# Performance work log

Hardware: AMD Instinct MI355X
Metric: run time of the kernel (lower is better)

Reference implementation:

```python
import jax, jax.numpy as jnp
import numpy as np

B, S, H, NH = 2, 2048, 1024, 16
HD = H // NH  # 64


def setup_inputs() -> dict:
    key = jax.random.key(0)
    ks = jax.random.split(key, 11)
    sc = 1.0 / np.sqrt(H)
    inp = {
        "q": jax.random.normal(ks[0], (B, S, H), dtype=jnp.float32),
        "k": jax.random.normal(ks[1], (B, S, H), dtype=jnp.float32),
        "v": jax.random.normal(ks[2], (B, S, H), dtype=jnp.float32),
        # nn.Linear params: weight [out,in], bias [out]
        "wq_w": jax.random.normal(ks[3], (H, H), dtype=jnp.float32) * sc,
        "wq_b": jnp.zeros((H,), dtype=jnp.float32),
        "wk_w": jax.random.normal(ks[4], (H, H), dtype=jnp.float32) * sc,
        "wk_b": jnp.zeros((H,), dtype=jnp.float32),
        "wv_w": jax.random.normal(ks[5], (H, H), dtype=jnp.float32) * sc,
        "wv_b": jnp.zeros((H,), dtype=jnp.float32),
        "wo_w": jax.random.normal(ks[6], (H, H), dtype=jnp.float32) * sc,
        "wo_b": jnp.zeros((H,), dtype=jnp.float32),
    }
    return inp


def _split_heads(x):
    # [B,S,H] -> [B,NH,S,HD]
    b, s, _ = x.shape
    return x.reshape(b, s, NH, HD).transpose(0, 2, 1, 3)


def reference(q, k, v, wq_w, wq_b, wk_w, wk_b, wv_w, wv_b, wo_w, wo_b):
    qw = q @ wq_w.T + wq_b
    kw = k @ wk_w.T + wk_b
    vw = v @ wv_w.T + wv_b
    hq = _split_heads(qw)  # [B,NH,S,HD]
    hk = _split_heads(kw)
    hv = _split_heads(vw)
    scale = 1.0 / jnp.sqrt(jnp.float32(HD))
    scores = jnp.einsum("bhqd,bhkd->bhqk", hq, hk) * scale  # [B,NH,S,S]
    attn = jax.nn.softmax(scores, axis=-1)
    out = jnp.einsum("bhqk,bhkd->bhqd", attn, hv)  # [B,NH,S,HD]
    out = out.transpose(0, 2, 1, 3).reshape(q.shape[0], -1, H)  # [B,S,H]
    final = out @ wo_w.T + wo_b
    return final, attn
```

## Files before the change

### kernel.cpp

```cpp
#include <hip/hip_runtime.h>

typedef short bf16x8 __attribute__((ext_vector_type(8)));
typedef float f32x4 __attribute__((ext_vector_type(4)));
typedef unsigned short ushort4v __attribute__((ext_vector_type(4)));
typedef unsigned short ushort8 __attribute__((ext_vector_type(8)));

#define DEVI static __device__ __forceinline__

DEVI unsigned short f2bf(float f) {
    unsigned u = __float_as_uint(f);
    u += 0x7FFFu + ((u >> 16) & 1u);
    return (unsigned short)(u >> 16);
}

DEVI unsigned cvtpk(float lo, float hi) {
    unsigned r;
    asm("v_cvt_pk_bf16_f32 %0, %1, %2" : "=v"(r) : "v"(lo), "v"(hi));
    return r;
}

typedef __attribute__((address_space(3))) unsigned int* lds_ptr_t;
typedef const __attribute__((address_space(1))) unsigned int* gbl_ptr_t;
#define GLDS(gp, lp) __builtin_amdgcn_global_load_lds((gbl_ptr_t)(gp), (lds_ptr_t)(lp), 16, 0, 0)

__global__ void cvt_kernel(const float* __restrict__ src, unsigned short* __restrict__ dst, int n) {
    int i = (blockIdx.x * 256 + threadIdx.x) * 4;
    if (i >= n) return;
    float4 v = *(const float4*)(src + i);
    ushort4v o;
    o.x = f2bf(v.x); o.y = f2bf(v.y); o.z = f2bf(v.z); o.w = f2bf(v.w);
    *(ushort4v*)(dst + i) = o;
}

__global__ void cvt2_kernel(const float* __restrict__ s0, unsigned short* __restrict__ d0, int n0,
                            const float* __restrict__ s1, unsigned short* __restrict__ d1, int n1) {
    int idx = blockIdx.x * 256 + threadIdx.x;
    const int c0 = n0 >> 2;
    const float* src; unsigned short* dst; int i;
    if (idx < c0) { src = s0; dst = d0; i = idx * 4; }
    else {
        i = (idx - c0) * 4;
        if (i >= n1) return;
        src = s1; dst = d1;
    }
    float4 v = *(const float4*)(src + i);
    ushort4v o;
    o.x = f2bf(v.x); o.y = f2bf(v.y); o.z = f2bf(v.z); o.w = f2bf(v.w);
    *(ushort4v*)(dst + i) = o;
}

template <int MODE>
__global__ __launch_bounds__(256) void gemm_bt(const unsigned short* __restrict__ A,
                                               const unsigned short* __restrict__ W,
                                               const float* __restrict__ bias,
                                               void* __restrict__ Cout) {
    constexpr int K = 1024;
    __shared__ unsigned short Asb[2][64 * 32];
    __shared__ unsigned short Bsb[2][128 * 32];
    const int t = threadIdx.x;
    const int w = t >> 6, l = t & 63;
    const int wr = w >> 1, wc = w & 1;
    const int fr = l & 15, fg = l >> 4;
    const int m0 = blockIdx.y * 64, n0 = blockIdx.x * 128;

    const int ra = t >> 2, qa = (t & 3) * 8;
    const int c1 = 256 + t, rb1 = c1 >> 2, qb1 = (c1 & 3) * 8;

    f32x4 acc[2][4] = {};

#define STG(kb, pb)                                                        \
    {                                                                      \
        GLDS(A + (size_t)(m0 + ra) * K + (kb) + qa, &Asb[pb][t * 8]);      \
        GLDS(W + (size_t)(n0 + ra) * K + (kb) + qa, &Bsb[pb][t * 8]);      \
        GLDS(W + (size_t)(n0 + rb1) * K + (kb) + qb1, &Bsb[pb][c1 * 8]);   \
    }

    STG(0, 0);
    for (int t2 = 0; t2 < 32; ++t2) {
        const int cur = t2 & 1;
        if (t2 < 31) {
            STG((t2 + 1) * 32, cur ^ 1);
            asm volatile("s_waitcnt vmcnt(3)" ::: "memory");
        } else {
            asm volatile("s_waitcnt vmcnt(0)" ::: "memory");
        }
        __syncthreads();
        bf16x8 af[2], bfv[4];
#pragma unroll
        for (int mi = 0; mi < 2; mi++)
            af[mi] = *(const bf16x8*)(&Asb[cur][(wr * 32 + mi * 16 + fr) * 32 + fg * 8]);
#pragma unroll
        for (int ni = 0; ni < 4; ni++)
            bfv[ni] = *(const bf16x8*)(&Bsb[cur][(wc * 64 + ni * 16 + fr) * 32 + fg * 8]);
#pragma unroll
        for (int mi = 0; mi < 2; mi++)
#pragma unroll
            for (int ni = 0; ni < 4; ni++)
                acc[mi][ni] = __builtin_amdgcn_mfma_f32_16x16x32_bf16(af[mi], bfv[ni], acc[mi][ni], 0, 0, 0);
        __syncthreads();
    }
#undef STG

#pragma unroll
    for (int ni = 0; ni < 4; ni++) {
        const int n = n0 + wc * 64 + ni * 16 + fr;
        const float bv = bias[n];
#pragma unroll
        for (int mi = 0; mi < 2; mi++) {
            const int mb = m0 + wr * 32 + mi * 16 + fg * 4;
            if constexpr (MODE == 1) {
                float* C = (float*)Cout;
#pragma unroll
                for (int r = 0; r < 4; r++) C[(size_t)(mb + r) * 1024 + n] = acc[mi][ni][r] + bv;
            } else if constexpr (MODE == 0) {
                unsigned short* C = (unsigned short*)Cout;
                const int h = n >> 6, hd = n & 63;
#pragma unroll
                for (int r = 0; r < 4; r++) {
                    const int m = mb + r;
                    const int bb = m >> 11, s = m & 2047;
                    C[(size_t)((bb * 16 + h) * 2048 + s) * 64 + hd] = f2bf(acc[mi][ni][r] + bv);
                }
            } else {
                unsigned short* C = (unsigned short*)Cout;
                const int h = n >> 6, hd = n & 63;
                const int bb = mb >> 11, s = mb & 2047;
                const int blk = s >> 6, off = s & 63;
                const int pos = blk * 64 + (off >> 5) * 32 + ((off & 15) >> 2) * 8 + ((off >> 4) & 1) * 4;
                ushort4v pk;
                pk.x = f2bf(acc[mi][ni][0] + bv);
                pk.y = f2bf(acc[mi][ni][1] + bv);
                pk.z = f2bf(acc[mi][ni][2] + bv);
                pk.w = f2bf(acc[mi][ni][3] + bv);
                *(ushort4v*)(C + (size_t)((bb * 16 + h) * 64 + hd) * 2048 + pos) = pk;
            }
        }
    }
}

__global__ __launch_bounds__(256, 2) void attn_kernel(const unsigned short* __restrict__ Qh,
                                                      const unsigned short* __restrict__ Kh,
                                                      const unsigned short* __restrict__ Vt,
                                                      unsigned short* __restrict__ Obuf,
                                                      float* __restrict__ AttnOut) {
    __shared__ float rpart[32][4];
    __shared__ float rinv_s[32];
    __shared__ float ored[32][68];

    const int i = blockIdx.x;
    const int qt = i & 63, bh = i >> 6;
    const int b = bh >> 4, h = bh & 15;
    const int q0 = qt * 32;
    const int t = threadIdx.x, w = t >> 6, l = t & 63;
    const int fr = l & 15, fg = l >> 4;
    const float SCL = 0.1803368801111f;

    const unsigned short* qb = Qh + (size_t)(bh * 2048 + q0) * 64;
    bf16x8 qf[2][2];
#pragma unroll
    for (int qs = 0; qs < 2; qs++)
#pragma unroll
        for (int kc = 0; kc < 2; kc++)
            qf[qs][kc] = *(const bf16x8*)(qb + (size_t)(qs * 16 + fr) * 64 + kc * 32 + fg * 8);

    const unsigned short* kbase = Kh + ((size_t)bh * 2048 + w * 512) * 64;
    const unsigned short* vtb = Vt + (size_t)bh * 64 * 2048;

    unsigned p0[8][8], p1[8][8];
    float rs0 = 0.f, rs1 = 0.f;
#pragma unroll
    for (int kt = 0; kt < 8; ++kt) {
#pragma unroll
        for (int mt = 0; mt < 4; ++mt) {
            const unsigned short* kr = kbase + (size_t)(kt * 64 + mt * 16 + fr) * 64 + fg * 8;
            bf16x8 kf0 = *(const bf16x8*)kr;
            bf16x8 kf1 = *(const bf16x8*)(kr + 32);
            f32x4 d0 = {}, d1 = {};
            d0 = __builtin_amdgcn_mfma_f32_16x16x32_bf16(kf0, qf[0][0], d0, 0, 0, 0);
            d0 = __builtin_amdgcn_mfma_f32_16x16x32_bf16(kf1, qf[0][1], d0, 0, 0, 0);
            d1 = __builtin_amdgcn_mfma_f32_16x16x32_bf16(kf0, qf[1][0], d1, 0, 0, 0);
            d1 = __builtin_amdgcn_mfma_f32_16x16x32_bf16(kf1, qf[1][1], d1, 0, 0, 0);
            const float a0 = exp2f(d0[0] * SCL), a1 = exp2f(d0[1] * SCL);
            const float a2 = exp2f(d0[2] * SCL), a3 = exp2f(d0[3] * SCL);
            rs0 += (a0 + a1) + (a2 + a3);
            p0[kt][mt * 2] = cvtpk(a0, a1);
            p0[kt][mt * 2 + 1] = cvtpk(a2, a3);
            const float c0 = exp2f(d1[0] * SCL), c1 = exp2f(d1[1] * SCL);
            const float c2 = exp2f(d1[2] * SCL), c3 = exp2f(d1[3] * SCL);
            rs1 += (c0 + c1) + (c2 + c3);
            p1[kt][mt * 2] = cvtpk(c0, c1);
            p1[kt][mt * 2 + 1] = cvtpk(c2, c3);
        }
    }
    rs0 += __shfl_xor(rs0, 16, 64); rs0 += __shfl_xor(rs0, 32, 64);
    rs1 += __shfl_xor(rs1, 16, 64); rs1 += __shfl_xor(rs1, 32, 64);
    if (l < 16) { rpart[l][w] = rs0; rpart[l + 16][w] = rs1; }
    __syncthreads();
    for (int j = t; j < 32 * 68; j += 256) (&ored[0][0])[j] = 0.f;
    if (t < 32) rinv_s[t] = 1.0f / (rpart[t][0] + rpart[t][1] + rpart[t][2] + rpart[t][3]);
    __syncthreads();
    const float ri0 = rinv_s[fr], ri1 = rinv_s[16 + fr];

    float* attnB0 = AttnOut + (size_t)bh * 2048 * 2048 + (size_t)(q0 + fr) * 2048 + w * 512;
    float* attnB1 = attnB0 + (size_t)16 * 2048;
    f32x4 opv[2][4] = {};
#pragma unroll
    for (int kt = 0; kt < 8; ++kt) {
#pragma unroll
        for (int mt = 0; mt < 4; ++mt) {
            const unsigned a = p0[kt][mt * 2], aa = p0[kt][mt * 2 + 1];
            f32x4 o;
            o[0] = __uint_as_float(a << 16) * ri0;
            o[1] = __uint_as_float(a & 0xffff0000u) * ri0;
            o[2] = __uint_as_float(aa << 16) * ri0;
            o[3] = __uint_as_float(aa & 0xffff0000u) * ri0;
            __builtin_nontemporal_store(o, (f32x4*)(attnB0 + kt * 64 + mt * 16 + fg * 4));
            const unsigned c = p1[kt][mt * 2], cc = p1[kt][mt * 2 + 1];
            f32x4 o1;
            o1[0] = __uint_as_float(c << 16) * ri1;
            o1[1] = __uint_as_float(c & 0xffff0000u) * ri1;
            o1[2] = __uint_as_float(cc << 16) * ri1;
            o1[3] = __uint_as_float(cc & 0xffff0000u) * ri1;
            __builtin_nontemporal_store(o1, (f32x4*)(attnB1 + kt * 64 + mt * 16 + fg * 4));
        }
#pragma unroll
        for (int kc = 0; kc < 2; ++kc) {
            union { unsigned u[4]; bf16x8 v; } pb0, pb1;
#pragma unroll
            for (int j = 0; j < 4; j++) { pb0.u[j] = p0[kt][4 * kc + j]; pb1.u[j] = p1[kt][4 * kc + j]; }
#pragma unroll
            for (int dt = 0; dt < 4; ++dt) {
                bf16x8 vf = *(const bf16x8*)(vtb + (size_t)(dt * 16 + fr) * 2048 + w * 512 + kt * 64 + kc * 32 + fg * 8);
                opv[0][dt] = __builtin_amdgcn_mfma_f32_16x16x32_bf16(vf, pb0.v, opv[0][dt], 0, 0, 0);
                opv[1][dt] = __builtin_amdgcn_mfma_f32_16x16x32_bf16(vf, pb1.v, opv[1][dt], 0, 0, 0);
            }
        }
    }

    __syncthreads();
    for (int ww = 0; ww < 4; ++ww) {
        if (w == ww) {
#pragma unroll
            for (int qs = 0; qs < 2; qs++)
#pragma unroll
                for (int dt = 0; dt < 4; dt++)
#pragma unroll
                    for (int r = 0; r < 4; r++)
                        ored[qs * 16 + fr][dt * 16 + 4 * fg + r] += opv[qs][dt][r];
        }
        __syncthreads();
    }
    {
        const int row = t >> 3, cb = (t & 7) * 8;
        const float rr = rinv_s[row];
        ushort8 pk;
#pragma unroll
        for (int j = 0; j < 8; j++) pk[j] = f2bf(ored[row][cb + j] * rr);
        *(ushort8*)(Obuf + (size_t)(b * 2048 + q0 + row) * 1024 + h * 64 + cb) = pk;
    }
}

extern "C" void kernel_launch(void* const* d_in, const int* in_sizes, int n_in,
                              void* d_out, int out_size, void* d_ws, size_t ws_size,
                              hipStream_t stream) {
    const float* q = (const float*)d_in[0];
    const float* k = (const float*)d_in[1];
    const float* v = (const float*)d_in[2];
    const float* wqw = (const float*)d_in[3];
    const float* wqb = (const float*)d_in[4];
    const float* wkw = (const float*)d_in[5];
    const float* wkb = (const float*)d_in[6];
    const float* wvw = (const float*)d_in[7];
    const float* wvb = (const float*)d_in[8];
    const float* wow = (const float*)d_in[9];
    const float* wob = (const float*)d_in[10];

    char* ws = (char*)d_ws;
    unsigned short* xbf  = (unsigned short*)(ws);
    unsigned short* wbf  = (unsigned short*)(ws + 8388608);
    unsigned short* qh   = (unsigned short*)(ws + 10485760);
    unsigned short* kh   = (unsigned short*)(ws + 18874368);
    unsigned short* vt   = (unsigned short*)(ws + 27262976);
    unsigned short* obuf = (unsigned short*)(ws + 35651584);

    float* finalOut = (float*)d_out;
    float* attnOut = finalOut + 4194304;

    const int NX = 4194304, NW = 1048576;
    const int c2grid = (NX + NW) / 1024;
    dim3 gGrid(8, 64);

    cvt2_kernel<<<c2grid, 256, 0, stream>>>(q, xbf, NX, wqw, wbf, NW);
    gemm_bt<0><<<gGrid, 256, 0, stream>>>(xbf, wbf, wqb, qh);

    cvt2_kernel<<<c2grid, 256, 0, stream>>>(k, xbf, NX, wkw, wbf, NW);
    gemm_bt<0><<<gGrid, 256, 0, stream>>>(xbf, wbf, wkb, kh);

    cvt2_kernel<<<c2grid, 256, 0, stream>>>(v, xbf, NX, wvw, wbf, NW);
    gemm_bt<2><<<gGrid, 256, 0, stream>>>(xbf, wbf, wvb, vt);

    attn_kernel<<<2048, 256, 0, stream>>>(qh, kh, vt, obuf, attnOut);

    cvt_kernel<<<NW / 1024, 256, 0, stream>>>(wow, wbf, NW);
    gemm_bt<1><<<gGrid, 256, 0, stream>>>(obuf, wbf, wob, finalOut);
}
```

Baseline: 301.9 us.

## Batch all conversions and QKV projections into single launches when workspace allows

When the workspace holds at least 64 MiB, the seven fp32-to-bf16 conversions are merged into one kernel and the three Q/K/V projection GEMMs into one 3D-grid launch, which cuts nine launches to four and lets the three GEMMs run concurrently for better device fill. The attention kernel also loads all V fragments for a key tile up front, before the attention-probability stores and MFMAs, to hide load latency. The cost is extra workspace, a fallback path kept for small workspaces, and more registers held for the V fragments.

```diff
diff --git a/kernel.cpp b/kernel.cpp
--- a/kernel.cpp
+++ b/kernel.cpp
@@ -49,58 +49,73 @@
     *(ushort4v*)(dst + i) = o;
 }
 
+__global__ void cvt4_kernel(const float* __restrict__ q, const float* __restrict__ k,
+                            const float* __restrict__ v, const float* __restrict__ wq,
+                            const float* __restrict__ wk, const float* __restrict__ wv,
+                            const float* __restrict__ wo, unsigned short* __restrict__ dq,
+                            unsigned short* __restrict__ dk, unsigned short* __restrict__ dv,
+                            unsigned short* __restrict__ dwq, unsigned short* __restrict__ dwk,
+                            unsigned short* __restrict__ dwv, unsigned short* __restrict__ dwo) {
+    int idx = blockIdx.x * 256 + threadIdx.x;
+    const float* src; unsigned short* dst; int base;
+    if (idx < 1048576) { src = q; dst = dq; base = idx; }
+    else if (idx < 2097152) { src = k; dst = dk; base = idx - 1048576; }
+    else if (idx < 3145728) { src = v; dst = dv; base = idx - 2097152; }
+    else if (idx < 3407872) { src = wq; dst = dwq; base = idx - 3145728; }
+    else if (idx < 3670016) { src = wk; dst = dwk; base = idx - 3407872; }
+    else if (idx < 3932160) { src = wv; dst = dwv; base = idx - 3670016; }
+    else { src = wo; dst = dwo; base = idx - 3932160; }
+    const int i = base * 4;
+    float4 x = *(const float4*)(src + i);
+    ushort4v o;
+    o.x = f2bf(x.x); o.y = f2bf(x.y); o.z = f2bf(x.z); o.w = f2bf(x.w);
+    *(ushort4v*)(dst + i) = o;
+}
+
+#define GEMM_BODY(A, W)                                                                             \
+    constexpr int K = 1024;                                                                         \
+    __shared__ unsigned short Asb[2][64 * 32];                                                      \
+    __shared__ unsigned short Bsb[2][128 * 32];                                                     \
+    const int t = threadIdx.x;                                                                      \
+    const int w = t >> 6, l = t & 63;                                                               \
+    const int wr = w >> 1, wc = w & 1;                                                              \
+    const int fr = l & 15, fg = l >> 4;                                                             \
+    const int m0 = blockIdx.y * 64, n0 = blockIdx.x * 128;                                          \
+    const int ra = t >> 2, qa = (t & 3) * 8;                                                        \
+    const int c1 = 256 + t, rb1 = c1 >> 2, qb1 = (c1 & 3) * 8;                                      \
+    f32x4 acc[2][4] = {};                                                                           \
+    GLDS(A + (size_t)(m0 + ra) * K + qa, &Asb[0][t * 8]);                                           \
+    GLDS(W + (size_t)(n0 + ra) * K + qa, &Bsb[0][t * 8]);                                           \
+    GLDS(W + (size_t)(n0 + rb1) * K + qb1, &Bsb[0][c1 * 8]);                                        \
+    for (int t2 = 0; t2 < 32; ++t2) {                                                               \
+        const int cur = t2 & 1;                                                                     \
+        if (t2 < 31) {                                                                              \
+            const int kb = (t2 + 1) * 32;                                                           \
+            GLDS(A + (size_t)(m0 + ra) * K + kb + qa, &Asb[cur ^ 1][t * 8]);                        \
+            GLDS(W + (size_t)(n0 + ra) * K + kb + qa, &Bsb[cur ^ 1][t * 8]);                        \
+            GLDS(W + (size_t)(n0 + rb1) * K + kb + qb1, &Bsb[cur ^ 1][c1 * 8]);                     \
+            asm volatile("s_waitcnt vmcnt(3)" ::: "memory");                                        \
+        } else {                                                                                    \
+            asm volatile("s_waitcnt vmcnt(0)" ::: "memory");                                        \
+        }                                                                                           \
+        __syncthreads();                                                                            \
+        bf16x8 af[2], bfv[4];                                                                       \
+        _Pragma("unroll") for (int mi = 0; mi < 2; mi++)                                            \
+            af[mi] = *(const bf16x8*)(&Asb[cur][(wr * 32 + mi * 16 + fr) * 32 + fg * 8]);           \
+        _Pragma("unroll") for (int ni = 0; ni < 4; ni++)                                            \
+            bfv[ni] = *(const bf16x8*)(&Bsb[cur][(wc * 64 + ni * 16 + fr) * 32 + fg * 8]);          \
+        _Pragma("unroll") for (int mi = 0; mi < 2; mi++)                                            \
+            _Pragma("unroll") for (int ni = 0; ni < 4; ni++)                                        \
+                acc[mi][ni] = __builtin_amdgcn_mfma_f32_16x16x32_bf16(af[mi], bfv[ni], acc[mi][ni], 0, 0, 0); \
+        __syncthreads();                                                                            \
+    }
+
 template <int MODE>
 __global__ __launch_bounds__(256) void gemm_bt(const unsigned short* __restrict__ A,
                                                const unsigned short* __restrict__ W,
                                                const float* __restrict__ bias,
                                                void* __restrict__ Cout) {
-    constexpr int K = 1024;
-    __shared__ unsigned short Asb[2][64 * 32];
-    __shared__ unsigned short Bsb[2][128 * 32];
-    const int t = threadIdx.x;
-    const int w = t >> 6, l = t & 63;
-    const int wr = w >> 1, wc = w & 1;
-    const int fr = l & 15, fg = l >> 4;
-    const int m0 = blockIdx.y * 64, n0 = blockIdx.x * 128;
-
-    const int ra = t >> 2, qa = (t & 3) * 8;
-    const int c1 = 256 + t, rb1 = c1 >> 2, qb1 = (c1 & 3) * 8;
-
-    f32x4 acc[2][4] = {};
-
-#define STG(kb, pb)                                                        \
-    {                                                                      \
-        GLDS(A + (size_t)(m0 + ra) * K + (kb) + qa, &Asb[pb][t * 8]);      \
-        GLDS(W + (size_t)(n0 + ra) * K + (kb) + qa, &Bsb[pb][t * 8]);      \
-        GLDS(W + (size_t)(n0 + rb1) * K + (kb) + qb1, &Bsb[pb][c1 * 8]);   \
-    }
-
-    STG(0, 0);
-    for (int t2 = 0; t2 < 32; ++t2) {
-        const int cur = t2 & 1;
-        if (t2 < 31) {
-            STG((t2 + 1) * 32, cur ^ 1);
-            asm volatile("s_waitcnt vmcnt(3)" ::: "memory");
-        } else {
-            asm volatile("s_waitcnt vmcnt(0)" ::: "memory");
-        }
-        __syncthreads();
-        bf16x8 af[2], bfv[4];
-#pragma unroll
-        for (int mi = 0; mi < 2; mi++)
-            af[mi] = *(const bf16x8*)(&Asb[cur][(wr * 32 + mi * 16 + fr) * 32 + fg * 8]);
-#pragma unroll
-        for (int ni = 0; ni < 4; ni++)
-            bfv[ni] = *(const bf16x8*)(&Bsb[cur][(wc * 64 + ni * 16 + fr) * 32 + fg * 8]);
-#pragma unroll
-        for (int mi = 0; mi < 2; mi++)
-#pragma unroll
-            for (int ni = 0; ni < 4; ni++)
-                acc[mi][ni] = __builtin_amdgcn_mfma_f32_16x16x32_bf16(af[mi], bfv[ni], acc[mi][ni], 0, 0, 0);
-        __syncthreads();
-    }
-#undef STG
-
+    GEMM_BODY(A, W)
 #pragma unroll
     for (int ni = 0; ni < 4; ni++) {
         const int n = n0 + wc * 64 + ni * 16 + fr;
@@ -133,6 +148,54 @@
                 pk.z = f2bf(acc[mi][ni][2] + bv);
                 pk.w = f2bf(acc[mi][ni][3] + bv);
                 *(ushort4v*)(C + (size_t)((bb * 16 + h) * 64 + hd) * 2048 + pos) = pk;
+            }
+        }
+    }
+}
+
+__global__ __launch_bounds__(256) void gemm_qkv(const unsigned short* __restrict__ Aq,
+                                                const unsigned short* __restrict__ Ak,
+                                                const unsigned short* __restrict__ Av,
+                                                const unsigned short* __restrict__ Wq,
+                                                const unsigned short* __restrict__ Wk,
+                                                const unsigned short* __restrict__ Wv,
+                                                const float* __restrict__ bq,
+                                                const float* __restrict__ bk,
+                                                const float* __restrict__ bv_,
+                                                unsigned short* __restrict__ qh,
+                                                unsigned short* __restrict__ kh,
+                                                unsigned short* __restrict__ vt) {
+    const int z = blockIdx.z;
+    const unsigned short* A = (z == 0) ? Aq : (z == 1) ? Ak : Av;
+    const unsigned short* W = (z == 0) ? Wq : (z == 1) ? Wk : Wv;
+    const float* bias = (z == 0) ? bq : (z == 1) ? bk : bv_;
+    GEMM_BODY(A, W)
+#pragma unroll
+    for (int ni = 0; ni < 4; ni++) {
+        const int n = n0 + wc * 64 + ni * 16 + fr;
+        const float bv = bias[n];
+        const int h = n >> 6, hd = n & 63;
+#pragma unroll
+        for (int mi = 0; mi < 2; mi++) {
+            const int mb = m0 + wr * 32 + mi * 16 + fg * 4;
+            if (z == 2) {
+                const int bb = mb >> 11, s = mb & 2047;
+                const int blk = s >> 6, off = s & 63;
+                const int pos = blk * 64 + (off >> 5) * 32 + ((off & 15) >> 2) * 8 + ((off >> 4) & 1) * 4;
+                ushort4v pk;
+                pk.x = f2bf(acc[mi][ni][0] + bv);
+                pk.y = f2bf(acc[mi][ni][1] + bv);
+                pk.z = f2bf(acc[mi][ni][2] + bv);
+                pk.w = f2bf(acc[mi][ni][3] + bv);
+                *(ushort4v*)(vt + (size_t)((bb * 16 + h) * 64 + hd) * 2048 + pos) = pk;
+            } else {
+                unsigned short* C = (z == 0) ? qh : kh;
+#pragma unroll
+                for (int r = 0; r < 4; r++) {
+                    const int m = mb + r;
+                    const int bb = m >> 11, s = m & 2047;
+                    C[(size_t)((bb * 16 + h) * 2048 + s) * 64 + hd] = f2bf(acc[mi][ni][r] + bv);
+                }
             }
         }
     }
@@ -206,6 +269,12 @@
     f32x4 opv[2][4] = {};
 #pragma unroll
     for (int kt = 0; kt < 8; ++kt) {
+        bf16x8 vf[2][4];
+#pragma unroll
+        for (int kc = 0; kc < 2; ++kc)
+#pragma unroll
+            for (int dt = 0; dt < 4; ++dt)
+                vf[kc][dt] = *(const bf16x8*)(vtb + (size_t)(dt * 16 + fr) * 2048 + w * 512 + kt * 64 + kc * 32 + fg * 8);
 #pragma unroll
         for (int mt = 0; mt < 4; ++mt) {
             const unsigned a = p0[kt][mt * 2], aa = p0[kt][mt * 2 + 1];
@@ -230,9 +299,8 @@
             for (int j = 0; j < 4; j++) { pb0.u[j] = p0[kt][4 * kc + j]; pb1.u[j] = p1[kt][4 * kc + j]; }
 #pragma unroll
             for (int dt = 0; dt < 4; ++dt) {
-                bf16x8 vf = *(const bf16x8*)(vtb + (size_t)(dt * 16 + fr) * 2048 + w * 512 + kt * 64 + kc * 32 + fg * 8);
-                opv[0][dt] = __builtin_amdgcn_mfma_f32_16x16x32_bf16(vf, pb0.v, opv[0][dt], 0, 0, 0);
-                opv[1][dt] = __builtin_amdgcn_mfma_f32_16x16x32_bf16(vf, pb1.v, opv[1][dt], 0, 0, 0);
+                opv[0][dt] = __builtin_amdgcn_mfma_f32_16x16x32_bf16(vf[kc][dt], pb0.v, opv[0][dt], 0, 0, 0);
+                opv[1][dt] = __builtin_amdgcn_mfma_f32_16x16x32_bf16(vf[kc][dt], pb1.v, opv[1][dt], 0, 0, 0);
             }
         }
     }
@@ -275,32 +343,50 @@
     const float* wow = (const float*)d_in[9];
     const float* wob = (const float*)d_in[10];
 
-    char* ws = (char*)d_ws;
-    unsigned short* xbf  = (unsigned short*)(ws);
-    unsigned short* wbf  = (unsigned short*)(ws + 8388608);
-    unsigned short* qh   = (unsigned short*)(ws + 10485760);
-    unsigned short* kh   = (unsigned short*)(ws + 18874368);
-    unsigned short* vt   = (unsigned short*)(ws + 27262976);
-    unsigned short* obuf = (unsigned short*)(ws + 35651584);
-
     float* finalOut = (float*)d_out;
     float* attnOut = finalOut + 4194304;
+    char* ws = (char*)d_ws;
 
     const int NX = 4194304, NW = 1048576;
-    const int c2grid = (NX + NW) / 1024;
     dim3 gGrid(8, 64);
 
-    cvt2_kernel<<<c2grid, 256, 0, stream>>>(q, xbf, NX, wqw, wbf, NW);
-    gemm_bt<0><<<gGrid, 256, 0, stream>>>(xbf, wbf, wqb, qh);
-
-    cvt2_kernel<<<c2grid, 256, 0, stream>>>(k, xbf, NX, wkw, wbf, NW);
-    gemm_bt<0><<<gGrid, 256, 0, stream>>>(xbf, wbf, wkb, kh);
-
-    cvt2_kernel<<<c2grid, 256, 0, stream>>>(v, xbf, NX, wvw, wbf, NW);
-    gemm_bt<2><<<gGrid, 256, 0, stream>>>(xbf, wbf, wvb, vt);
-
-    attn_kernel<<<2048, 256, 0, stream>>>(qh, kh, vt, obuf, attnOut);
-
-    cvt_kernel<<<NW / 1024, 256, 0, stream>>>(wow, wbf, NW);
-    gemm_bt<1><<<gGrid, 256, 0, stream>>>(obuf, wbf, wob, finalOut);
-}
+    if (ws_size >= 67108864ull) {
+        unsigned short* qbf  = (unsigned short*)(ws);
+        unsigned short* kbf  = (unsigned short*)(ws + 8388608);
+        unsigned short* vbf  = (unsigned short*)(ws + 16777216);
+        unsigned short* wqbf = (unsigned short*)(ws + 25165824);
+        unsigned short* wkbf = (unsigned short*)(ws + 27262976);
+        unsigned short* wvbf = (unsigned short*)(ws + 29360128);
+        unsigned short* wobf = (unsigned short*)(ws + 31457280);
+        unsigned short* qh   = (unsigned short*)(ws + 33554432);
+        unsigned short* kh   = (unsigned short*)(ws + 41943040);
+        unsigned short* vt   = (unsigned short*)(ws + 50331648);
+        unsigned short* obuf = (unsigned short*)(ws + 58720256);
+
+        cvt4_kernel<<<16384, 256, 0, stream>>>(q, k, v, wqw, wkw, wvw, wow,
+                                               qbf, kbf, vbf, wqbf, wkbf, wvbf, wobf);
+        dim3 g3(8, 64, 3);
+        gemm_qkv<<<g3, 256, 0, stream>>>(qbf, kbf, vbf, wqbf, wkbf, wvbf,
+                                         wqb, wkb, wvb, qh, kh, vt);
+        attn_kernel<<<2048, 256, 0, stream>>>(qh, kh, vt, obuf, attnOut);
+        gemm_bt<1><<<gGrid, 256, 0, stream>>>(obuf, wobf, wob, finalOut);
+    } else {
+        unsigned short* xbf  = (unsigned short*)(ws);
+        unsigned short* wbf  = (unsigned short*)(ws + 8388608);
+        unsigned short* qh   = (unsigned short*)(ws + 10485760);
+        unsigned short* kh   = (unsigned short*)(ws + 18874368);
+        unsigned short* vt   = (unsigned short*)(ws + 27262976);
+        unsigned short* obuf = (unsigned short*)(ws + 35651584);
+        const int c2grid = (NX + NW) / 1024;
+
+        cvt2_kernel<<<c2grid, 256, 0, stream>>>(q, xbf, NX, wqw, wbf, NW);
+        gemm_bt<0><<<gGrid, 256, 0, stream>>>(xbf, wbf, wqb, qh);
+        cvt2_kernel<<<c2grid, 256, 0, stream>>>(k, xbf, NX, wkw, wbf, NW);
+        gemm_bt<0><<<gGrid, 256, 0, stream>>>(xbf, wbf, wkb, kh);
+        cvt2_kernel<<<c2grid, 256, 0, stream>>>(v, xbf, NX, wvw, wbf, NW);
+        gemm_bt<2><<<gGrid, 256, 0, stream>>>(xbf, wbf, wvb, vt);
+        attn_kernel<<<2048, 256, 0, stream>>>(qh, kh, vt, obuf, attnOut);
+        cvt_kernel<<<NW / 1024, 256, 0, stream>>>(wow, wbf, NW);
+        gemm_bt<1><<<gGrid, 256, 0, stream>>>(obuf, wbf, wob, finalOut);
+    }
+}
```

Result: faster. 283.5 us (-6.1%).
